# Optimization experiments

Hardware: AMD Instinct MI355X
Metric: run time of the kernel (lower is better)

The kernel has to match this reference:

```python
import jax, jax.numpy as jnp
import numpy as np
import math


def _cnot_perm(n, c, t):
    # permutation on basis states implementing CNOT(control=c, target=t), qubit 0 = MSB
    idx = np.arange(2 ** n)
    ctrl = (idx >> (n - 1 - c)) & 1
    return np.where(ctrl == 1, idx ^ (1 << (n - 1 - t)), idx)


def _rot(phi, theta, omega):
    # PennyLane Rot(phi, theta, omega) = RZ(omega) RY(theta) RZ(phi)
    c = jnp.cos(theta / 2.0)
    s = jnp.sin(theta / 2.0)
    m00 = jnp.exp(-0.5j * (phi + omega)) * c
    m01 = -jnp.exp(0.5j * (phi - omega)) * s
    m10 = jnp.exp(-0.5j * (phi - omega)) * s
    m11 = jnp.exp(0.5j * (phi + omega)) * c
    return jnp.stack([jnp.stack([m00, m01]), jnp.stack([m10, m11])])


def _apply_1q(state, U, q, n):
    # apply 2x2 gate U on qubit q of an [N, 2^n] statevector
    N = state.shape[0]
    s = state.reshape(N, 2 ** q, 2, 2 ** (n - q - 1))
    s = jnp.einsum('ab,nqbr->nqar', U, s)
    return s.reshape(N, 2 ** n)


def reference(x, weights, bias, filter_size, strides):
    fs, st = int(filter_size), int(strides)
    B, C, H, W = x.shape
    Cout, L, n, _ = weights.shape
    oh = (H - fs) // st + 1
    ow = (W - fs) // st + 1

    # im2col / torch.unfold: [B,C,oh,fs,ow,fs] -> [B,oh,ow,C,fs,fs] -> [N, C*fs*fs]
    rows = (jnp.arange(oh) * st)[:, None] + jnp.arange(fs)[None, :]
    cols = (jnp.arange(ow) * st)[:, None] + jnp.arange(fs)[None, :]
    patches = x[:, :, rows][:, :, :, :, cols]                 # [B,C,oh,fs,ow,fs]
    patches = patches.transpose(0, 2, 4, 1, 3, 5).reshape(B * oh * ow, C * fs * fs)

    D = C * fs * fs
    dim = 2 ** n
    if D < dim:
        patches = jnp.pad(patches, ((0, 0), (0, dim - D)))

    # amplitude-encoding normalization; all-zero patch vectors are masked to 0 output
    norm = jnp.linalg.norm(patches, axis=-1, keepdims=True)
    nonzero = (norm[:, 0] > 0).astype(patches.dtype)          # [N]
    state0 = (patches / jnp.where(norm > 0, norm, 1.0)).astype(jnp.complex64)

    perms = [jnp.asarray(_cnot_perm(n, q, (q + 1) % n)) for q in range(n)]
    sign = (1.0 - 2.0 * ((jnp.arange(dim) >> (n - 1)) & 1)).astype(jnp.float32)  # Z on qubit 0

    def run_channel(wc):  # wc: [L, n, 3]
        state = state0
        for l in range(L):
            for q in range(n):
                state = _apply_1q(state, _rot(wc[l, q, 0], wc[l, q, 1], wc[l, q, 2]), q, n)
            if n > 1:
                for q in range(n):  # CNOT ring
                    state = state[:, perms[q]]
        return jnp.sum((jnp.abs(state) ** 2) * sign, axis=-1)  # [N] expval Z0

    exps = jax.vmap(run_channel)(weights)                     # [Cout, N]
    out = exps * nonzero[None, :] + bias[:, None]
    return out.reshape(Cout, B, oh, ow).transpose(1, 0, 2, 3)


def setup_inputs() -> dict:
    key = jax.random.key(0)
    k1, k2, k3 = jax.random.split(key, 3)
    B, Cin, H, W = 32, 16, 64, 64
    Cout, L, fs, st = 8, 3, 4, 2
    D = Cin * fs * fs
    n = math.ceil(math.log2(D))
    x = jax.random.normal(k1, (B, Cin, H, W), dtype=jnp.float32)
    weights = jax.random.normal(k2, (Cout, L, n, 3), dtype=jnp.float32)
    kk = 1.0 / D
    bias = jax.random.uniform(k3, (Cout,), minval=-math.sqrt(kk), maxval=math.sqrt(kk), dtype=jnp.float32)
    return {"x": x, "weights": weights, "bias": bias, "filter_size": fs, "strides": st}
```

## Files before the change

### kernel.cpp

```cpp
#include <hip/hip_runtime.h>
#include <math.h>

#define NQ     8
#define DIM    256
#define LAYERS 3
#define COUT   8
#define NB     32
#define OH     31
#define OW     31
#define NPATCH (NB*OH*OW)
#define PT_BLK 512
#define NTILE  64
#define PTOT   (NTILE*PT_BLK)
#define NPTILE (PTOT/16)
#define NPAIR  72
#define MPACK  (NPAIR*64*8)

typedef _Float16 f16x8 __attribute__((ext_vector_type(8)));
typedef _Float16 f16x4 __attribute__((ext_vector_type(4)));
typedef float    f32x4 __attribute__((ext_vector_type(4)));

__device__ __forceinline__ float2 cmul(float2 a, float2 b) {
    return make_float2(a.x*b.x - a.y*b.y, a.x*b.y + a.y*b.x);
}
__device__ __forceinline__ float2 cadd(float2 a, float2 b) {
    return make_float2(a.x + b.x, a.y + b.y);
}

__device__ __forceinline__ int rho(int i) {
    #pragma unroll
    for (int q = 7; q >= 0; --q) {
        int t = (q + 1) & 7;
        if ((i >> (7 - q)) & 1) i ^= 1 << (7 - t);
    }
    return i;
}

__global__ __launch_bounds__(256) void build_W(const float* __restrict__ w,
                                               _Float16* __restrict__ At,
                                               _Float16* __restrict__ Bt) {
    const int j  = blockIdx.x;
    const int ch = blockIdx.y;
    const int i  = threadIdx.x;
    __shared__ float2 g[96];
    __shared__ float2 v[256];
    if (i < 24) {
        const float* wp = w + (ch*24 + i)*3;
        float phi = wp[0], th = wp[1], om = wp[2];
        float cth = cosf(th * 0.5f), sth = sinf(th * 0.5f);
        float a = 0.5f * (phi + om), b = 0.5f * (phi - om);
        float sa, ca, sb, cb;
        sincosf(a, &sa, &ca);
        sincosf(b, &sb, &cb);
        g[i*4+0] = make_float2( cth*ca, -cth*sa);
        g[i*4+1] = make_float2(-sth*cb, -sth*sb);
        g[i*4+2] = make_float2( sth*cb, -sth*sb);
        g[i*4+3] = make_float2( cth*ca,  cth*sa);
    }
    __syncthreads();

    float2 acc = make_float2(1.f, 0.f);
    #pragma unroll
    for (int q = 0; q < 8; ++q) {
        int iq = (i >> (7 - q)) & 1, jq = (j >> (7 - q)) & 1;
        acc = cmul(acc, g[q*4 + iq*2 + jq]);
    }
    v[i] = acc;
    __syncthreads();

    #pragma unroll
    for (int l = 1; l < 3; ++l) {
        float2 a = v[rho(i)];
        __syncthreads();
        v[i] = a;
        __syncthreads();
        #pragma unroll
        for (int q = 0; q < 8; ++q) {
            int bit = 1 << (7 - q);
            float2 m00 = g[(l*8+q)*4+0], m01 = g[(l*8+q)*4+1];
            float2 m10 = g[(l*8+q)*4+2], m11 = g[(l*8+q)*4+3];
            float2 x = v[i], y = v[i ^ bit];
            __syncthreads();
            float2 nv = (i & bit) ? cadd(cmul(m10, y), cmul(m11, x))
                                  : cadd(cmul(m00, x), cmul(m01, y));
            v[i] = nv;
            __syncthreads();
        }
    }
    float2 a = v[rho(i)];
    float sgn = (i & 128) ? -1.f : 1.f;
    size_t row = ((size_t)ch*256 + j) * 512;
    At[row + i]       = (_Float16)(sgn * a.x);
    At[row + 256 + i] = (_Float16)(sgn * a.y);
    Bt[row + i]       = (_Float16)a.x;
    Bt[row + 256 + i] = (_Float16)a.y;
}

__global__ __launch_bounds__(256) void build_Mp(const _Float16* __restrict__ At,
                                                const _Float16* __restrict__ Bt,
                                                _Float16* __restrict__ Mp) {
    const int ch = blockIdx.z;
    const int ti = blockIdx.y;
    const int wv = threadIdx.x >> 6;
    const int jt = blockIdx.x * 4 + wv;
    const int jt0 = 2 * (ti >> 1);
    if (jt < jt0) return;
    const int lane = threadIdx.x & 63;
    const int c16 = lane & 15, kq = lane >> 4;
    const int OFFT[16] = {0,8,16,23,30,36,42,47,52,56,60,63,66,68,70,71};
    const int pidx = OFFT[ti] + (jt >> 1) - (ti >> 1);
    _Float16* Mc = Mp + (size_t)ch * MPACK;

    f32x4 acc = {0.f, 0.f, 0.f, 0.f};
    if (jt >= ti) {
        const _Float16* Ar = At + ((size_t)ch*256 + ti*16 + c16) * 512 + kq*8;
        const _Float16* Br = Bt + ((size_t)ch*256 + jt*16 + c16) * 512 + kq*8;
        #pragma unroll
        for (int kk = 0; kk < 16; ++kk) {
            f16x8 af = *(const f16x8*)(Ar + kk*32);
            f16x8 bf = *(const f16x8*)(Br + kk*32);
            acc = __builtin_amdgcn_mfma_f32_16x16x32_f16(af, bf, acc, 0, 0, 0);
        }
    }
    int wsel = (jt & 1) * 16 + c16;
    int kqp = wsel >> 3, jj = wsel & 7;
    #pragma unroll
    for (int reg = 0; reg < 4; ++reg) {
        int i_g = ti*16 + kq*4 + reg;
        int j_g = jt*16 + c16;
        float val = (jt >= ti) ? acc[reg] : 0.f;
        val *= (j_g > i_g) ? 2.f : ((j_g == i_g) ? 1.f : 0.f);
        Mc[(size_t)((pidx*64 + kqp*16 + (kq*4 + reg)) * 8 + jj)] = (_Float16)val;
    }
}

__global__ __launch_bounds__(256) void extract(const float* __restrict__ x,
                                               _Float16* __restrict__ sF) {
    const int tb  = blockIdx.x;
    const int tid = threadIdx.x;
    const int wv  = tid >> 6, lane = tid & 63;
    __shared__ _Float16 sT[16][264];

    #pragma unroll
    for (int pp = 0; pp < 4; ++pp) {
        int pl = wv*4 + pp;
        int p  = tb*16 + pl;
        float2 v01 = make_float2(0.f,0.f), v23 = make_float2(0.f,0.f);
        if (p < NPATCH) {
            int b = p / (OH*OW); int r = p % (OH*OW);
            int oi = r / OW, oj = r % OW;
            int ci = lane >> 2, fi = lane & 3;
            const float* xb = x + (((size_t)(b*16 + ci))*64 + (oi*2 + fi))*64 + oj*2;
            v01 = *(const float2*)xb;
            v23 = *(const float2*)(xb + 2);
        }
        float ss = v01.x*v01.x + v01.y*v01.y + v23.x*v23.x + v23.y*v23.y;
        #pragma unroll
        for (int m = 1; m < 64; m <<= 1) ss += __shfl_xor(ss, m, 64);
        float inv = ss > 0.f ? 1.f / sqrtf(ss) : 0.f;
        f16x4 o;
        o[0] = (_Float16)(v01.x*inv); o[1] = (_Float16)(v01.y*inv);
        o[2] = (_Float16)(v23.x*inv); o[3] = (_Float16)(v23.y*inv);
        *(f16x4*)&sT[pl][lane*4] = o;
    }
    __syncthreads();

    #pragma unroll
    for (int e = 0; e < 2; ++e) {
        int vi = tid + e*256;
        int ks = vi >> 6, ln = vi & 63;
        int kq = ln >> 4, prow = ln & 15;
        f16x8 o = *(const f16x8*)&sT[prow][ks*32 + kq*8];
        ((f16x8*)sF)[(size_t)tb*512 + vi] = o;
    }
}

__global__ __attribute__((amdgpu_flat_work_group_size(512,512), amdgpu_waves_per_eu(2,2)))
void fusedqf(const _Float16* __restrict__ sF,
             const _Float16* __restrict__ Mp,
             const float* __restrict__ bias,
             float* __restrict__ out) {
    extern __shared__ _Float16 Mlds[];
    const int id   = blockIdx.x;
    const int xcd  = id & 7;
    const int g    = id >> 3;
    const int c    = g >> 3;
    const int tile = (g & 7) * 8 + xcd;
    const int tid  = threadIdx.x;
    const int lane = tid & 63;
    const int wv   = tid >> 6;
    const int prow = lane & 15, kq = lane >> 4;
    const int tp0  = tile*32 + wv*4;

    const _Float16* Msrc = Mp + (size_t)c * MPACK;
    #pragma unroll
    for (int it = 0; it < 9; ++it) {
        int vi = it * 512 + tid;
        ((f16x8*)Mlds)[vi] = ((const f16x8*)Msrc)[vi];
    }

    f16x8 bfrag[4][8];
    #pragma unroll
    for (int pt = 0; pt < 4; ++pt) {
        const f16x8* src = (const f16x8*)sF + (size_t)(tp0 + pt)*512 + lane;
        #pragma unroll
        for (int ks = 0; ks < 8; ++ks)
            bfrag[pt][ks] = src[ks*64];
    }

    __syncthreads();

    const _Float16* fold0[4];
    #pragma unroll
    for (int pt = 0; pt < 4; ++pt)
        fold0[pt] = sF + ((size_t)(tp0 + pt)*8*64 + (kq>>1)*16 + prow)*8 + (kq&1)*4;

    float o0 = 0.f, o1 = 0.f, o2 = 0.f, o3 = 0.f;
    int pidx = 0;

    #pragma unroll 2
    for (int t = 0; t < 16; ++t) {
        f32x4 a0 = {0,0,0,0}, a1 = {0,0,0,0}, a2 = {0,0,0,0}, a3 = {0,0,0,0};
        #pragma unroll
        for (int ks = 0; ks < 8; ++ks) {
            if (ks >= (t >> 1)) {
                f16x8 a = *(const f16x8*)(Mlds + pidx*512 + lane*8);
                a0 = __builtin_amdgcn_mfma_f32_16x16x32_f16(a, bfrag[0][ks], a0, 0, 0, 0);
                a1 = __builtin_amdgcn_mfma_f32_16x16x32_f16(a, bfrag[1][ks], a1, 0, 0, 0);
                a2 = __builtin_amdgcn_mfma_f32_16x16x32_f16(a, bfrag[2][ks], a2, 0, 0, 0);
                a3 = __builtin_amdgcn_mfma_f32_16x16x32_f16(a, bfrag[3][ks], a3, 0, 0, 0);
                ++pidx;
            }
        }
        {
            f16x4 sv = *(const f16x4*)(fold0[0] + t*256);
            o0 += (float)sv[0]*a0[0] + (float)sv[1]*a0[1] + (float)sv[2]*a0[2] + (float)sv[3]*a0[3];
        }
        {
            f16x4 sv = *(const f16x4*)(fold0[1] + t*256);
            o1 += (float)sv[0]*a1[0] + (float)sv[1]*a1[1] + (float)sv[2]*a1[2] + (float)sv[3]*a1[3];
        }
        {
            f16x4 sv = *(const f16x4*)(fold0[2] + t*256);
            o2 += (float)sv[0]*a2[0] + (float)sv[1]*a2[1] + (float)sv[2]*a2[2] + (float)sv[3]*a2[3];
        }
        {
            f16x4 sv = *(const f16x4*)(fold0[3] + t*256);
            o3 += (float)sv[0]*a3[0] + (float)sv[1]*a3[1] + (float)sv[2]*a3[2] + (float)sv[3]*a3[3];
        }
    }

    float ov[4] = {o0, o1, o2, o3};
    float bc = bias[c];
    #pragma unroll
    for (int pt = 0; pt < 4; ++pt) {
        float v = ov[pt];
        v += __shfl_xor(v, 16, 64);
        v += __shfl_xor(v, 32, 64);
        if (kq == 0) {
            int p = (tp0 + pt)*16 + prow;
            if (p < NPATCH) {
                int b = p / (OH*OW); int r2 = p % (OH*OW);
                int oi = r2 / OW, oj = r2 % OW;
                out[(((size_t)(b*COUT + c))*OH + oi)*OW + oj] = v + bc;
            }
        }
    }
}

extern "C" void kernel_launch(void* const* d_in, const int* in_sizes, int n_in,
                              void* d_out, int out_size, void* d_ws, size_t ws_size,
                              hipStream_t stream) {
    const float* x    = (const float*)d_in[0];
    const float* w    = (const float*)d_in[1];
    const float* bias = (const float*)d_in[2];
    float* out = (float*)d_out;

    const size_t OFF_AT  = 0;
    const size_t OFF_BT  = OFF_AT + 2097152;
    const size_t OFF_MP  = OFF_BT + 2097152;
    const size_t OFF_SF  = OFF_MP + 589824;
    const size_t TOTAL   = OFF_SF + 16777216;
    if (ws_size < TOTAL) return;

    char* ws = (char*)d_ws;
    _Float16* At = (_Float16*)(ws + OFF_AT);
    _Float16* Bt = (_Float16*)(ws + OFF_BT);
    _Float16* Mp = (_Float16*)(ws + OFF_MP);
    _Float16* sF = (_Float16*)(ws + OFF_SF);

    build_W<<<dim3(256, COUT), 256, 0, stream>>>(w, At, Bt);
    build_Mp<<<dim3(4, 16, COUT), 256, 0, stream>>>(At, Bt, Mp);
    extract<<<NPTILE, 256, 0, stream>>>(x, sF);
    fusedqf<<<NTILE*COUT, 512, MPACK*sizeof(_Float16), stream>>>(sF, Mp, bias, out);
}
```

Baseline: 62.24 us.

## Fuse weight build with patch extraction and unroll main loop with prefetch

Merges the build_W and extract kernels into a single launch, with block ranges selecting the role, which removes one kernel launch and lets the two independent stages overlap. Inside the weight build, six of the eight per-qubit gate applications now exchange values with wavefront shuffles instead of going through shared memory with barriers. In the main fused kernel the t loop is fully unrolled with compile-time pack indices, and the fold-vector loads for the next iteration are prefetched. The cost is more register pressure and larger code in the hot kernel.

```diff
diff --git a/kernel.cpp b/kernel.cpp
--- a/kernel.cpp
+++ b/kernel.cpp
@@ -36,64 +36,111 @@
     return i;
 }
 
-__global__ __launch_bounds__(256) void build_W(const float* __restrict__ w,
-                                               _Float16* __restrict__ At,
-                                               _Float16* __restrict__ Bt) {
-    const int j  = blockIdx.x;
-    const int ch = blockIdx.y;
-    const int i  = threadIdx.x;
+__global__ __launch_bounds__(256) void wext(const float* __restrict__ w,
+                                            _Float16* __restrict__ At,
+                                            _Float16* __restrict__ Bt,
+                                            const float* __restrict__ x,
+                                            _Float16* __restrict__ sF) {
     __shared__ float2 g[96];
-    __shared__ float2 v[256];
-    if (i < 24) {
-        const float* wp = w + (ch*24 + i)*3;
-        float phi = wp[0], th = wp[1], om = wp[2];
-        float cth = cosf(th * 0.5f), sth = sinf(th * 0.5f);
-        float a = 0.5f * (phi + om), b = 0.5f * (phi - om);
-        float sa, ca, sb, cb;
-        sincosf(a, &sa, &ca);
-        sincosf(b, &sb, &cb);
-        g[i*4+0] = make_float2( cth*ca, -cth*sa);
-        g[i*4+1] = make_float2(-sth*cb, -sth*sb);
-        g[i*4+2] = make_float2( sth*cb, -sth*sb);
-        g[i*4+3] = make_float2( cth*ca,  cth*sa);
-    }
-    __syncthreads();
-
-    float2 acc = make_float2(1.f, 0.f);
-    #pragma unroll
-    for (int q = 0; q < 8; ++q) {
-        int iq = (i >> (7 - q)) & 1, jq = (j >> (7 - q)) & 1;
-        acc = cmul(acc, g[q*4 + iq*2 + jq]);
-    }
-    v[i] = acc;
-    __syncthreads();
-
-    #pragma unroll
-    for (int l = 1; l < 3; ++l) {
-        float2 a = v[rho(i)];
+    __shared__ float2 vb[256];
+    __shared__ _Float16 sT[16][264];
+
+    if (blockIdx.x < 2048) {
+        const int j  = blockIdx.x & 255;
+        const int ch = blockIdx.x >> 8;
+        const int i  = threadIdx.x;
+        if (i < 24) {
+            const float* wp = w + (ch*24 + i)*3;
+            float phi = wp[0], th = wp[1], om = wp[2];
+            float cth = cosf(th * 0.5f), sth = sinf(th * 0.5f);
+            float a = 0.5f * (phi + om), b = 0.5f * (phi - om);
+            float sa, ca, sb, cb;
+            sincosf(a, &sa, &ca);
+            sincosf(b, &sb, &cb);
+            g[i*4+0] = make_float2( cth*ca, -cth*sa);
+            g[i*4+1] = make_float2(-sth*cb, -sth*sb);
+            g[i*4+2] = make_float2( sth*cb, -sth*sb);
+            g[i*4+3] = make_float2( cth*ca,  cth*sa);
+        }
         __syncthreads();
-        v[i] = a;
+
+        float2 v = make_float2(1.f, 0.f);
+        #pragma unroll
+        for (int q = 0; q < 8; ++q) {
+            int iq = (i >> (7 - q)) & 1, jq = (j >> (7 - q)) & 1;
+            v = cmul(v, g[q*4 + iq*2 + jq]);
+        }
+
+        #pragma unroll
+        for (int l = 1; l < 3; ++l) {
+            vb[i] = v; __syncthreads();
+            v = vb[rho(i)]; __syncthreads();
+            #pragma unroll
+            for (int q = 0; q < 2; ++q) {
+                int bit = 1 << (7 - q);
+                vb[i] = v; __syncthreads();
+                float2 y = vb[i ^ bit]; __syncthreads();
+                float2 m0 = (i & bit) ? g[(l*8+q)*4+3] : g[(l*8+q)*4+0];
+                float2 m1 = (i & bit) ? g[(l*8+q)*4+2] : g[(l*8+q)*4+1];
+                v = cadd(cmul(m0, v), cmul(m1, y));
+            }
+            #pragma unroll
+            for (int q = 2; q < 8; ++q) {
+                int bit = 1 << (7 - q);
+                float2 y;
+                y.x = __shfl_xor(v.x, bit, 64);
+                y.y = __shfl_xor(v.y, bit, 64);
+                float2 m0 = (i & bit) ? g[(l*8+q)*4+3] : g[(l*8+q)*4+0];
+                float2 m1 = (i & bit) ? g[(l*8+q)*4+2] : g[(l*8+q)*4+1];
+                v = cadd(cmul(m0, v), cmul(m1, y));
+            }
+        }
+        vb[i] = v; __syncthreads();
+        float2 a = vb[rho(i)];
+        float sgn = (i & 128) ? -1.f : 1.f;
+        size_t row = ((size_t)ch*256 + j) * 512;
+        At[row + i]       = (_Float16)(sgn * a.x);
+        At[row + 256 + i] = (_Float16)(sgn * a.y);
+        Bt[row + i]       = (_Float16)a.x;
+        Bt[row + 256 + i] = (_Float16)a.y;
+    } else {
+        const int tb  = blockIdx.x - 2048;
+        const int tid = threadIdx.x;
+        const int wv  = tid >> 6, lane = tid & 63;
+
+        #pragma unroll
+        for (int pp = 0; pp < 4; ++pp) {
+            int pl = wv*4 + pp;
+            int p  = tb*16 + pl;
+            float2 v01 = make_float2(0.f,0.f), v23 = make_float2(0.f,0.f);
+            if (p < NPATCH) {
+                int b = p / (OH*OW); int r = p % (OH*OW);
+                int oi = r / OW, oj = r % OW;
+                int ci = lane >> 2, fi = lane & 3;
+                const float* xb = x + (((size_t)(b*16 + ci))*64 + (oi*2 + fi))*64 + oj*2;
+                v01 = *(const float2*)xb;
+                v23 = *(const float2*)(xb + 2);
+            }
+            float ss = v01.x*v01.x + v01.y*v01.y + v23.x*v23.x + v23.y*v23.y;
+            #pragma unroll
+            for (int m = 1; m < 64; m <<= 1) ss += __shfl_xor(ss, m, 64);
+            float inv = ss > 0.f ? 1.f / sqrtf(ss) : 0.f;
+            f16x4 o;
+            o[0] = (_Float16)(v01.x*inv); o[1] = (_Float16)(v01.y*inv);
+            o[2] = (_Float16)(v23.x*inv); o[3] = (_Float16)(v23.y*inv);
+            *(f16x4*)&sT[pl][lane*4] = o;
+        }
         __syncthreads();
-        #pragma unroll
-        for (int q = 0; q < 8; ++q) {
-            int bit = 1 << (7 - q);
-            float2 m00 = g[(l*8+q)*4+0], m01 = g[(l*8+q)*4+1];
-            float2 m10 = g[(l*8+q)*4+2], m11 = g[(l*8+q)*4+3];
-            float2 x = v[i], y = v[i ^ bit];
-            __syncthreads();
-            float2 nv = (i & bit) ? cadd(cmul(m10, y), cmul(m11, x))
-                                  : cadd(cmul(m00, x), cmul(m01, y));
-            v[i] = nv;
-            __syncthreads();
-        }
-    }
-    float2 a = v[rho(i)];
-    float sgn = (i & 128) ? -1.f : 1.f;
-    size_t row = ((size_t)ch*256 + j) * 512;
-    At[row + i]       = (_Float16)(sgn * a.x);
-    At[row + 256 + i] = (_Float16)(sgn * a.y);
-    Bt[row + i]       = (_Float16)a.x;
-    Bt[row + 256 + i] = (_Float16)a.y;
+
+        #pragma unroll
+        for (int e = 0; e < 2; ++e) {
+            int vi = tid + e*256;
+            int ks = vi >> 6, ln = vi & 63;
+            int kq = ln >> 4, prow = ln & 15;
+            f16x8 o = *(const f16x8*)&sT[prow][ks*32 + kq*8];
+            ((f16x8*)sF)[(size_t)tb*512 + vi] = o;
+        }
+    }
 }
 
 __global__ __launch_bounds__(256) void build_Mp(const _Float16* __restrict__ At,
@@ -131,47 +178,6 @@
         float val = (jt >= ti) ? acc[reg] : 0.f;
         val *= (j_g > i_g) ? 2.f : ((j_g == i_g) ? 1.f : 0.f);
         Mc[(size_t)((pidx*64 + kqp*16 + (kq*4 + reg)) * 8 + jj)] = (_Float16)val;
-    }
-}
-
-__global__ __launch_bounds__(256) void extract(const float* __restrict__ x,
-                                               _Float16* __restrict__ sF) {
-    const int tb  = blockIdx.x;
-    const int tid = threadIdx.x;
-    const int wv  = tid >> 6, lane = tid & 63;
-    __shared__ _Float16 sT[16][264];
-
-    #pragma unroll
-    for (int pp = 0; pp < 4; ++pp) {
-        int pl = wv*4 + pp;
-        int p  = tb*16 + pl;
-        float2 v01 = make_float2(0.f,0.f), v23 = make_float2(0.f,0.f);
-        if (p < NPATCH) {
-            int b = p / (OH*OW); int r = p % (OH*OW);
-            int oi = r / OW, oj = r % OW;
-            int ci = lane >> 2, fi = lane & 3;
-            const float* xb = x + (((size_t)(b*16 + ci))*64 + (oi*2 + fi))*64 + oj*2;
-            v01 = *(const float2*)xb;
-            v23 = *(const float2*)(xb + 2);
-        }
-        float ss = v01.x*v01.x + v01.y*v01.y + v23.x*v23.x + v23.y*v23.y;
-        #pragma unroll
-        for (int m = 1; m < 64; m <<= 1) ss += __shfl_xor(ss, m, 64);
-        float inv = ss > 0.f ? 1.f / sqrtf(ss) : 0.f;
-        f16x4 o;
-        o[0] = (_Float16)(v01.x*inv); o[1] = (_Float16)(v01.y*inv);
-        o[2] = (_Float16)(v23.x*inv); o[3] = (_Float16)(v23.y*inv);
-        *(f16x4*)&sT[pl][lane*4] = o;
-    }
-    __syncthreads();
-
-    #pragma unroll
-    for (int e = 0; e < 2; ++e) {
-        int vi = tid + e*256;
-        int ks = vi >> 6, ln = vi & 63;
-        int kq = ln >> 4, prow = ln & 15;
-        f16x8 o = *(const f16x8*)&sT[prow][ks*32 + kq*8];
-        ((f16x8*)sF)[(size_t)tb*512 + vi] = o;
     }
 }
 
@@ -210,44 +216,41 @@
 
     __syncthreads();
 
-    const _Float16* fold0[4];
+    const _Float16* fold0 = sF + ((size_t)tp0*512 + (kq>>1)*16 + prow)*8 + (kq&1)*4;
+
+    float o0 = 0.f, o1 = 0.f, o2 = 0.f, o3 = 0.f;
+
+    f16x4 svn[4];
     #pragma unroll
     for (int pt = 0; pt < 4; ++pt)
-        fold0[pt] = sF + ((size_t)(tp0 + pt)*8*64 + (kq>>1)*16 + prow)*8 + (kq&1)*4;
-
-    float o0 = 0.f, o1 = 0.f, o2 = 0.f, o3 = 0.f;
-    int pidx = 0;
-
-    #pragma unroll 2
+        svn[pt] = *(const f16x4*)(fold0 + pt*4096);
+
+    #pragma unroll
     for (int t = 0; t < 16; ++t) {
+        f16x4 svc[4];
+        #pragma unroll
+        for (int pt = 0; pt < 4; ++pt) svc[pt] = svn[pt];
+        if (t < 15) {
+            #pragma unroll
+            for (int pt = 0; pt < 4; ++pt)
+                svn[pt] = *(const f16x4*)(fold0 + pt*4096 + (t+1)*256);
+        }
+
         f32x4 a0 = {0,0,0,0}, a1 = {0,0,0,0}, a2 = {0,0,0,0}, a3 = {0,0,0,0};
         #pragma unroll
-        for (int ks = 0; ks < 8; ++ks) {
-            if (ks >= (t >> 1)) {
-                f16x8 a = *(const f16x8*)(Mlds + pidx*512 + lane*8);
-                a0 = __builtin_amdgcn_mfma_f32_16x16x32_f16(a, bfrag[0][ks], a0, 0, 0, 0);
-                a1 = __builtin_amdgcn_mfma_f32_16x16x32_f16(a, bfrag[1][ks], a1, 0, 0, 0);
-                a2 = __builtin_amdgcn_mfma_f32_16x16x32_f16(a, bfrag[2][ks], a2, 0, 0, 0);
-                a3 = __builtin_amdgcn_mfma_f32_16x16x32_f16(a, bfrag[3][ks], a3, 0, 0, 0);
-                ++pidx;
-            }
-        }
-        {
-            f16x4 sv = *(const f16x4*)(fold0[0] + t*256);
-            o0 += (float)sv[0]*a0[0] + (float)sv[1]*a0[1] + (float)sv[2]*a0[2] + (float)sv[3]*a0[3];
-        }
-        {
-            f16x4 sv = *(const f16x4*)(fold0[1] + t*256);
-            o1 += (float)sv[0]*a1[0] + (float)sv[1]*a1[1] + (float)sv[2]*a1[2] + (float)sv[3]*a1[3];
-        }
-        {
-            f16x4 sv = *(const f16x4*)(fold0[2] + t*256);
-            o2 += (float)sv[0]*a2[0] + (float)sv[1]*a2[1] + (float)sv[2]*a2[2] + (float)sv[3]*a2[3];
-        }
-        {
-            f16x4 sv = *(const f16x4*)(fold0[3] + t*256);
-            o3 += (float)sv[0]*a3[0] + (float)sv[1]*a3[1] + (float)sv[2]*a3[2] + (float)sv[3]*a3[3];
-        }
+        for (int ks = (t >> 1); ks < 8; ++ks) {
+            const int OFFT[16] = {0,8,16,23,30,36,42,47,52,56,60,63,66,68,70,71};
+            int pidx = OFFT[t] + ks - (t >> 1);
+            f16x8 a = *(const f16x8*)(Mlds + pidx*512 + lane*8);
+            a0 = __builtin_amdgcn_mfma_f32_16x16x32_f16(a, bfrag[0][ks], a0, 0, 0, 0);
+            a1 = __builtin_amdgcn_mfma_f32_16x16x32_f16(a, bfrag[1][ks], a1, 0, 0, 0);
+            a2 = __builtin_amdgcn_mfma_f32_16x16x32_f16(a, bfrag[2][ks], a2, 0, 0, 0);
+            a3 = __builtin_amdgcn_mfma_f32_16x16x32_f16(a, bfrag[3][ks], a3, 0, 0, 0);
+        }
+        o0 += (float)svc[0][0]*a0[0] + (float)svc[0][1]*a0[1] + (float)svc[0][2]*a0[2] + (float)svc[0][3]*a0[3];
+        o1 += (float)svc[1][0]*a1[0] + (float)svc[1][1]*a1[1] + (float)svc[1][2]*a1[2] + (float)svc[1][3]*a1[3];
+        o2 += (float)svc[2][0]*a2[0] + (float)svc[2][1]*a2[1] + (float)svc[2][2]*a2[2] + (float)svc[2][3]*a2[3];
+        o3 += (float)svc[3][0]*a3[0] + (float)svc[3][1]*a3[1] + (float)svc[3][2]*a3[2] + (float)svc[3][3]*a3[3];
     }
 
     float ov[4] = {o0, o1, o2, o3};
@@ -289,8 +292,7 @@
     _Float16* Mp = (_Float16*)(ws + OFF_MP);
     _Float16* sF = (_Float16*)(ws + OFF_SF);
 
-    build_W<<<dim3(256, COUT), 256, 0, stream>>>(w, At, Bt);
+    wext<<<2048 + NPTILE, 256, 0, stream>>>(w, At, Bt, x, sF);
     build_Mp<<<dim3(4, 16, COUT), 256, 0, stream>>>(At, Bt, Mp);
-    extract<<<NPTILE, 256, 0, stream>>>(x, sF);
     fusedqf<<<NTILE*COUT, 512, MPACK*sizeof(_Float16), stream>>>(sF, Mp, bias, out);
 }
```

Result: slower. 65.44 us (+5.1%).
